# Kernel optimization log

Measured on AMD Instinct MI355X. Metric: run time of the kernel, lower is better.

## Reference

```python
import jax, jax.numpy as jnp
import numpy as np

V, D, T, H, L, B = 50257, 1024, 1024, 16, 6, 2
HS = D // H  # 64
EPS = 1e-5


def setup_inputs() -> dict:
    key = jax.random.key(0)
    ks = jax.random.split(key, 16)
    s = 0.02
    n = lambda k, sh: jax.random.normal(k, sh, jnp.float32) * s
    return {
        'idx': jax.random.randint(ks[0], (B, T), 0, V),
        'targets': jax.random.randint(ks[1], (B, T), 0, V),
        'tok_emb': n(ks[2], (V, D)),
        'pos_emb': n(ks[3], (T, D)),
        'wq': n(ks[4], (L, H, D, HS)),
        'wk': n(ks[5], (L, H, D, HS)),
        'wv': n(ks[6], (L, H, D, HS)),
        'wproj': n(ks[7], (L, D, D)),
        'bproj': jnp.zeros((L, D), jnp.float32),
        'ln1_g': jnp.ones((L, D), jnp.float32),
        'ln1_b': jnp.zeros((L, D), jnp.float32),
        'ln2_g': jnp.ones((L, D), jnp.float32),
        'ln2_b': jnp.zeros((L, D), jnp.float32),
        'w1': n(ks[8], (L, D, 4 * D)),
        'b1': jnp.zeros((L, 4 * D), jnp.float32),
        'w2': n(ks[9], (L, 4 * D, D)),
        'b2': jnp.zeros((L, D), jnp.float32),
        'lnf_g': jnp.ones((D,), jnp.float32),
        'lnf_b': jnp.zeros((D,), jnp.float32),
        'lm_w': n(ks[10], (D, V)),
        'lm_b': jnp.zeros((V,), jnp.float32),
    }


def _layernorm(x, g, b):
    mu = jnp.mean(x, axis=-1, keepdims=True)
    var = jnp.var(x, axis=-1, keepdims=True)
    return (x - mu) * jax.lax.rsqrt(var + EPS) * g + b


def _forward(idx, targets, tok_emb, pos_emb, wq, wk, wv, wproj, bproj,
             ln1_g, ln1_b, ln2_g, ln2_b, w1, b1, w2, b2, lnf_g, lnf_b, lm_w, lm_b):
    t = idx.shape[1]
    x = tok_emb[idx] + pos_emb[:t]  # [B,T,D]
    causal = jnp.tril(jnp.ones((t, t), bool))  # [T,T]
    neg_inf = jnp.float32(-jnp.inf)

    def block(x, p):
        (wq_l, wk_l, wv_l, wp_l, bp_l, g1, b1_ln, g2, b2_ln, wf1, bf1, wf2, bf2) = p
        h = _layernorm(x, g1, b1_ln)
        q = jnp.einsum('btd,hdk->bhtk', h, wq_l)
        k = jnp.einsum('btd,hdk->bhtk', h, wk_l)
        v = jnp.einsum('btd,hdk->bhtk', h, wv_l)
        scores = jnp.einsum('bhtk,bhsk->bhts', q, k) * (HS ** -0.5)
        scores = jnp.where(causal, scores, neg_inf)
        attn = jax.nn.softmax(scores, axis=-1)  # dropout p=0.0
        o = jnp.einsum('bhts,bhsk->bhtk', attn, v)
        o = o.transpose(0, 2, 1, 3).reshape(x.shape[0], t, H * HS)  # concat heads
        x = x + o @ wp_l + bp_l
        h2 = _layernorm(x, g2, b2_ln)
        x = x + jax.nn.relu(h2 @ wf1 + bf1) @ wf2 + bf2
        return x, None

    x, _ = jax.lax.scan(block, x, (wq, wk, wv, wproj, bproj,
                                   ln1_g, ln1_b, ln2_g, ln2_b, w1, b1, w2, b2))
    x = _layernorm(x, lnf_g, lnf_b)
    logits = x @ lm_w + lm_b  # [B,T,V]
    logp = jax.nn.log_softmax(logits, axis=-1)
    loss = -jnp.mean(jnp.take_along_axis(logp, targets[..., None], axis=-1))
    return logits, loss


def reference(idx, targets, tok_emb, pos_emb, wq, wk, wv, wproj, bproj,
              ln1_g, ln1_b, ln2_g, ln2_b, w1, b1, w2, b2, lnf_g, lnf_b, lm_w, lm_b):
    return _forward(idx, targets, tok_emb, pos_emb, wq, wk, wv, wproj, bproj,
                    ln1_g, ln1_b, ln2_g, ln2_b, w1, b1, w2, b2, lnf_g, lnf_b, lm_w, lm_b)
```

## Files before the change

kernel.cpp:

```cpp
#include <hip/hip_runtime.h>
#include <cstdint>
#include <cstddef>

typedef unsigned short u16;
typedef unsigned int u32;
typedef __bf16 bf16x8 __attribute__((ext_vector_type(8)));
typedef float f32x4 __attribute__((ext_vector_type(4)));
typedef short short8_t __attribute__((ext_vector_type(8)));

#define NV 50257
#define NVPAD 50304
#define NBLK_LM 393
#define PSTR 400
#define ND 1024
#define NT 1024
#define NH 16
#define NL 6
#define NB 2
#define NM 2048
#define NF 4096
#define EPSLN 1e-5f

__device__ __forceinline__ u16 f2bf(float f) {
    unsigned u = __float_as_uint(f);
    return (u16)((u + 0x7fffu + ((u >> 16) & 1u)) >> 16);
}
__device__ __forceinline__ float bf2f(u16 h) {
    return __uint_as_float(((unsigned)h) << 16);
}
__device__ __forceinline__ u32 pack2bf(float lo, float hi) {
    return (u32)f2bf(lo) | ((u32)f2bf(hi) << 16);
}

__device__ __forceinline__ void gload_lds16(const u16* g, u16* l) {
    __builtin_amdgcn_global_load_lds((const __attribute__((address_space(1))) void*)g,
                                     (__attribute__((address_space(3))) void*)l, 16, 0, 0);
}

__device__ __forceinline__ float wave_reduce_sum(float v) {
#pragma unroll
    for (int off = 32; off >= 1; off >>= 1) v += __shfl_xor(v, off, 64);
    return v;
}

__global__ __launch_bounds__(256) void k_embed(const int* __restrict__ idx,
                                               const float* __restrict__ tok,
                                               const float* __restrict__ pos,
                                               float* __restrict__ x) {
    int m = blockIdx.x;
    int t = m & (NT - 1);
    int tokid = idx[m];
    int d = threadIdx.x * 4;
    float4 a = *(const float4*)(tok + (size_t)tokid * ND + d);
    float4 p = *(const float4*)(pos + (size_t)t * ND + d);
    a.x += p.x; a.y += p.y; a.z += p.z; a.w += p.w;
    *(float4*)(x + (size_t)m * ND + d) = a;
}

__global__ __launch_bounds__(256) void k_layernorm(const float* __restrict__ x,
                                                   const float* __restrict__ g,
                                                   const float* __restrict__ b,
                                                   u16* __restrict__ outb) {
    int m = blockIdx.x;
    int d = threadIdx.x * 4;
    const float4 v = *(const float4*)(x + (size_t)m * ND + d);
    float s = v.x + v.y + v.z + v.w;
    float q = v.x * v.x + v.y * v.y + v.z * v.z + v.w * v.w;
    s = wave_reduce_sum(s);
    q = wave_reduce_sum(q);
    __shared__ float ss[4], sq[4];
    int lane = threadIdx.x & 63, w = threadIdx.x >> 6;
    if (lane == 0) { ss[w] = s; sq[w] = q; }
    __syncthreads();
    s = ss[0] + ss[1] + ss[2] + ss[3];
    q = sq[0] + sq[1] + sq[2] + sq[3];
    float mu = s * (1.0f / ND);
    float var = q * (1.0f / ND) - mu * mu;
    float rstd = rsqrtf(var + EPSLN);
    float4 gg = *(const float4*)(g + d);
    float4 bb = *(const float4*)(b + d);
    ushort4 pk;
    pk.x = f2bf((v.x - mu) * rstd * gg.x + bb.x);
    pk.y = f2bf((v.y - mu) * rstd * gg.y + bb.y);
    pk.z = f2bf((v.z - mu) * rstd * gg.z + bb.z);
    pk.w = f2bf((v.w - mu) * rstd * gg.w + bb.w);
    *(ushort4*)(outb + (size_t)m * ND + d) = pk;
}

__global__ __launch_bounds__(256) void k_wtrans(const float* __restrict__ W,
                                                u16* __restrict__ Wt,
                                                int K, int N, int Npad, int hs, int ld) {
    __shared__ float t[32][33];
    const int nb = blockIdx.x << 5, kb = blockIdx.y << 5;
    const int tx = threadIdx.x & 31, tq = threadIdx.x >> 5;
    const int n = nb + tx;
    if (n < N) {
        const int head = n / hs, nc = n - head * hs;
        const float* src = W + (size_t)head * K * hs + nc;
#pragma unroll
        for (int i = 0; i < 4; ++i)
            t[(tq << 2) + i][tx] = src[(size_t)(kb + (tq << 2) + i) * ld];
    } else {
#pragma unroll
        for (int i = 0; i < 4; ++i) t[(tq << 2) + i][tx] = 0.f;
    }
    __syncthreads();
#pragma unroll
    for (int i = 0; i < 4; ++i) {
        const int nn = nb + (tq << 2) + i;
        if (nn < Npad) Wt[(size_t)nn * K + kb + tx] = f2bf(t[tx][(tq << 2) + i]);
    }
}

__global__ __launch_bounds__(256) void k_wtrans_qkv(const float* __restrict__ Wq,
                                                    const float* __restrict__ Wk,
                                                    const float* __restrict__ Wv,
                                                    u16* __restrict__ Wt) {
    __shared__ float t[32][33];
    const float* W = (blockIdx.z == 0) ? Wq : (blockIdx.z == 1) ? Wk : Wv;
    u16* dst = Wt + (size_t)blockIdx.z * ND * ND;
    const int nb = blockIdx.x << 5, kb = blockIdx.y << 5;
    const int tx = threadIdx.x & 31, tq = threadIdx.x >> 5;
    const int n = nb + tx;
    {
        const int head = n >> 6, nc = n & 63;
        const float* src = W + (size_t)head * ND * 64 + nc;
#pragma unroll
        for (int i = 0; i < 4; ++i)
            t[(tq << 2) + i][tx] = src[(size_t)(kb + (tq << 2) + i) * 64];
    }
    __syncthreads();
#pragma unroll
    for (int i = 0; i < 4; ++i) {
        const int nn = nb + (tq << 2) + i;
        dst[(size_t)nn * ND + kb + tx] = f2bf(t[tx][(tq << 2) + i]);
    }
}

__global__ __launch_bounds__(256) void k_vtrans(const u16* __restrict__ qkv,
                                                u16* __restrict__ vt) {
    __shared__ u16 L[64][72];
    const int tt = blockIdx.x, bh = blockIdx.y;
    const int b = bh >> 4, h = bh & 15;
    const int tid = threadIdx.x;
    const int tr = tid >> 2, dc = (tid & 3) << 4;
    const u16* src = qkv + (size_t)(b * NT + tt * 64 + tr) * 3072 + 2048 + h * 64 + dc;
    short8_t v0 = *(const short8_t*)src;
    short8_t v1 = *(const short8_t*)(src + 8);
#pragma unroll
    for (int j = 0; j < 8; ++j) { L[tr][dc + j] = (u16)v0[j]; L[tr][dc + 8 + j] = (u16)v1[j]; }
    __syncthreads();
    const int dr = tid >> 2, tc = (tid & 3) << 4;
    union { u16 us[16]; short8_t v[2]; } tmp;
#pragma unroll
    for (int j = 0; j < 16; ++j) tmp.us[j] = L[tc + j][dr];
    u16* dst = vt + ((size_t)bh * 64 + dr) * NT + tt * 64 + tc;
    *(short8_t*)dst = tmp.v[0];
    *(short8_t*)(dst + 8) = tmp.v[1];
}

template <bool RELU, bool RESID, bool NBOUND, bool PART, bool OUTBF16>
__global__ __launch_bounds__(256) void k_mfma_gemm(
    const u16* __restrict__ A, const u16* __restrict__ Bt,
    const float* __restrict__ bias, const float* __restrict__ resid,
    float* __restrict__ Cf, u16* __restrict__ Cb,
    float* __restrict__ pmax_g, float* __restrict__ psum_g,
    int K, int N, int ldc)
{
    __shared__ u16 As[2][128 * 32];
    __shared__ u16 Bs[2][128 * 32];
    const int lin = blockIdx.y * 16 + blockIdx.x;
    const int nwg = (int)gridDim.y * 16;
    const int cpx = nwg >> 3;
    const int swz = (lin & 7) * cpx + (lin >> 3);
    const int m0 = (swz & 15) * 128;
    const int n0 = (swz >> 4) * 128;
    const int tid = threadIdx.x;
    const int lane = tid & 63, wv = tid >> 6;
    const int wr = wv >> 1, wc = wv & 1;
    const int lr = lane & 15, kg = lane >> 4;

    const int srow = lane >> 2;
    const int scol = (((lane & 3) ^ ((lane >> 3) & 3)) << 3);
    const u16* gA0 = A + (size_t)(m0 + wv * 16 + srow) * K + scol;
    const u16* gA1 = gA0 + (size_t)64 * K;
    const u16* gB0 = Bt + (size_t)(n0 + wv * 16 + srow) * K + scol;
    const u16* gB1 = gB0 + (size_t)64 * K;

    f32x4 acc[4][4] = {};
    const int nt = K >> 5;

    gload_lds16(gA0, &As[0][wv * 512]);
    gload_lds16(gA1, &As[0][2048 + wv * 512]);
    gload_lds16(gB0, &Bs[0][wv * 512]);
    gload_lds16(gB1, &Bs[0][2048 + wv * 512]);
    __syncthreads();

    int cur = 0;
    for (int t = 0; t < nt; ++t) {
        if (t + 1 < nt) {
            const int ko = (t + 1) << 5;
            gload_lds16(gA0 + ko, &As[cur ^ 1][wv * 512]);
            gload_lds16(gA1 + ko, &As[cur ^ 1][2048 + wv * 512]);
            gload_lds16(gB0 + ko, &Bs[cur ^ 1][wv * 512]);
            gload_lds16(gB1 + ko, &Bs[cur ^ 1][2048 + wv * 512]);
        }
        bf16x8 af[4], bfr[4];
        const int rsw = ((kg ^ ((lr >> 1) & 3)) << 3);
#pragma unroll
        for (int mi = 0; mi < 4; ++mi) {
            const int R = wr * 64 + mi * 16 + lr;
            af[mi] = *(const bf16x8*)&As[cur][R * 32 + rsw];
        }
#pragma unroll
        for (int ni = 0; ni < 4; ++ni) {
            const int R = wc * 64 + ni * 16 + lr;
            bfr[ni] = *(const bf16x8*)&Bs[cur][R * 32 + rsw];
        }
#pragma unroll
        for (int mi = 0; mi < 4; ++mi)
#pragma unroll
            for (int ni = 0; ni < 4; ++ni)
                acc[mi][ni] = __builtin_amdgcn_mfma_f32_16x16x32_bf16(af[mi], bfr[ni], acc[mi][ni], 0, 0, 0);
        __syncthreads();
        cur ^= 1;
    }
#pragma unroll
    for (int mi = 0; mi < 4; ++mi) {
#pragma unroll
        for (int ni = 0; ni < 4; ++ni) {
#pragma unroll
            for (int r = 0; r < 4; ++r) {
                const int row = m0 + wr * 64 + mi * 16 + kg * 4 + r;
                const int col = n0 + wc * 64 + ni * 16 + lr;
                if (NBOUND && col >= N) continue;
                float c = acc[mi][ni][r];
                if (bias) c += bias[col];
                if (RELU) c = fmaxf(c, 0.f);
                if (RESID) c += resid[(size_t)row * ldc + col];
                if (OUTBF16) Cb[(size_t)row * ldc + col] = f2bf(c);
                else         Cf[(size_t)row * ldc + col] = c;
            }
        }
    }
    if constexpr (PART) {
        __shared__ float redm[128][2];
        __shared__ float reds[128][2];
#pragma unroll
        for (int mi = 0; mi < 4; ++mi)
#pragma unroll
            for (int r = 0; r < 4; ++r) {
                float vmax = -3.0e38f;
#pragma unroll
                for (int ni = 0; ni < 4; ++ni) {
                    const int col = n0 + wc * 64 + ni * 16 + lr;
                    float c = acc[mi][ni][r] + ((col < N) ? bias[col] : 0.f);
                    if (col >= N) c = -3.0e38f;
                    vmax = fmaxf(vmax, c);
                }
                vmax = fmaxf(vmax, __shfl_xor(vmax, 1));
                vmax = fmaxf(vmax, __shfl_xor(vmax, 2));
                vmax = fmaxf(vmax, __shfl_xor(vmax, 4));
                vmax = fmaxf(vmax, __shfl_xor(vmax, 8));
                if (lr == 0) redm[wr * 64 + mi * 16 + kg * 4 + r][wc] = vmax;
            }
        __syncthreads();
#pragma unroll
        for (int mi = 0; mi < 4; ++mi)
#pragma unroll
            for (int r = 0; r < 4; ++r) {
                const int rloc = wr * 64 + mi * 16 + kg * 4 + r;
                const float M = fmaxf(redm[rloc][0], redm[rloc][1]);
                float s = 0.f;
#pragma unroll
                for (int ni = 0; ni < 4; ++ni) {
                    const int col = n0 + wc * 64 + ni * 16 + lr;
                    if (col < N) {
                        float c = acc[mi][ni][r] + bias[col];
                        s += __expf(c - M);
                    }
                }
                s += __shfl_xor(s, 1);
                s += __shfl_xor(s, 2);
                s += __shfl_xor(s, 4);
                s += __shfl_xor(s, 8);
                if (lr == 0) reds[rloc][wc] = s;
            }
        __syncthreads();
        if (tid < 128) {
            const float M = fmaxf(redm[tid][0], redm[tid][1]);
            const int nblk = n0 >> 7;
            pmax_g[(size_t)(m0 + tid) * PSTR + nblk] = M;
            psum_g[(size_t)(m0 + tid) * PSTR + nblk] = reds[tid][0] + reds[tid][1];
        }
    }
}

template <bool RELU, bool RESID, bool OUTBF16>
__global__ __launch_bounds__(256) void k_gemm_n64(
    const u16* __restrict__ A, const u16* __restrict__ Bt,
    const float* __restrict__ bias, const float* __restrict__ resid,
    float* __restrict__ Cf, u16* __restrict__ Cb,
    int K, int ldc)
{
    __shared__ u16 As[2][128 * 32];
    __shared__ u16 Bs[2][64 * 32];
    const int lin = blockIdx.y * 16 + blockIdx.x;
    const int nwg = (int)gridDim.y * 16;
    const int cpx = nwg >> 3;
    const int swz = (lin & 7) * cpx + (lin >> 3);
    const int m0 = (swz & 15) * 128;
    const int n0 = (swz >> 4) * 64;
    const int tid = threadIdx.x;
    const int lane = tid & 63, wv = tid >> 6;
    const int lr = lane & 15, kg = lane >> 4;

    const int srow = lane >> 2;
    const int scol = (((lane & 3) ^ ((lane >> 3) & 3)) << 3);
    const u16* gA0 = A + (size_t)(m0 + wv * 32 + srow) * K + scol;
    const u16* gA1 = gA0 + (size_t)16 * K;
    const u16* gB0 = Bt + (size_t)(n0 + wv * 16 + srow) * K + scol;

    f32x4 acc[2][4] = {};
    const int nt = K >> 5;

    gload_lds16(gA0, &As[0][wv * 1024]);
    gload_lds16(gA1, &As[0][wv * 1024 + 512]);
    gload_lds16(gB0, &Bs[0][wv * 512]);
    __syncthreads();

    int cur = 0;
    for (int t = 0; t < nt; ++t) {
        if (t + 1 < nt) {
            const int ko = (t + 1) << 5;
            gload_lds16(gA0 + ko, &As[cur ^ 1][wv * 1024]);
            gload_lds16(gA1 + ko, &As[cur ^ 1][wv * 1024 + 512]);
            gload_lds16(gB0 + ko, &Bs[cur ^ 1][wv * 512]);
        }
        bf16x8 af[2], bfr[4];
        const int rsw = ((kg ^ ((lr >> 1) & 3)) << 3);
#pragma unroll
        for (int mi = 0; mi < 2; ++mi)
            af[mi] = *(const bf16x8*)&As[cur][(wv * 32 + mi * 16 + lr) * 32 + rsw];
#pragma unroll
        for (int ni = 0; ni < 4; ++ni)
            bfr[ni] = *(const bf16x8*)&Bs[cur][(ni * 16 + lr) * 32 + rsw];
#pragma unroll
        for (int mi = 0; mi < 2; ++mi)
#pragma unroll
            for (int ni = 0; ni < 4; ++ni)
                acc[mi][ni] = __builtin_amdgcn_mfma_f32_16x16x32_bf16(af[mi], bfr[ni], acc[mi][ni], 0, 0, 0);
        __syncthreads();
        cur ^= 1;
    }
#pragma unroll
    for (int mi = 0; mi < 2; ++mi) {
#pragma unroll
        for (int ni = 0; ni < 4; ++ni) {
#pragma unroll
            for (int r = 0; r < 4; ++r) {
                const int row = m0 + wv * 32 + mi * 16 + kg * 4 + r;
                const int col = n0 + ni * 16 + lr;
                float c = acc[mi][ni][r];
                if (bias) c += bias[col];
                if (RELU) c = fmaxf(c, 0.f);
                if (RESID) c += resid[(size_t)row * ldc + col];
                if (OUTBF16) Cb[(size_t)row * ldc + col] = f2bf(c);
                else         Cf[(size_t)row * ldc + col] = c;
            }
        }
    }
}

__global__ __launch_bounds__(256) void k_attn_mfma(const u16* __restrict__ qkv,
                                                   const u16* __restrict__ vt,
                                                   u16* __restrict__ ob) {
    const int qt = blockIdx.x, bh = blockIdx.y;
    const int b = bh >> 4, h = bh & 15;
    const int tid = threadIdx.x;
    const int lane = tid & 63, w = tid >> 6;
    const int lr = lane & 15, kg = lane >> 4;

    __shared__ u16 Qs[64 * 64];
    __shared__ u16 Ks[2][64 * 64];
    __shared__ u16 Vs[2][64 * 64];

    const int srow8 = lane >> 3;
    const int csw = ((lane & 7) ^ srow8) << 3;

    {
        const int r0 = w * 8 + srow8;
        gload_lds16(qkv + (size_t)(b * NT + qt * 64 + r0) * 3072 + h * 64 + csw, &Qs[w * 512]);
        gload_lds16(qkv + (size_t)(b * NT + qt * 64 + 32 + r0) * 3072 + h * 64 + csw, &Qs[2048 + w * 512]);
    }
#define STAGE_KV(bb, st)                                                                            \
    {                                                                                               \
        const int r0_ = w * 8 + srow8;                                                              \
        gload_lds16(qkv + (size_t)(b * NT + (st) * 64 + r0_) * 3072 + 1024 + h * 64 + csw,          \
                    &Ks[bb][w * 512]);                                                              \
        gload_lds16(qkv + (size_t)(b * NT + (st) * 64 + 32 + r0_) * 3072 + 1024 + h * 64 + csw,     \
                    &Ks[bb][2048 + w * 512]);                                                       \
        gload_lds16(vt + ((size_t)bh * 64 + r0_) * NT + (st) * 64 + csw, &Vs[bb][w * 512]);         \
        gload_lds16(vt + ((size_t)bh * 64 + 32 + r0_) * NT + (st) * 64 + csw,                       \
                    &Vs[bb][2048 + w * 512]);                                                       \
    }
    STAGE_KV(0, 0);
    __syncthreads();

    bf16x8 qf[2];
    {
        const int qrow = w * 16 + lr;
#pragma unroll
        for (int ds_ = 0; ds_ < 2; ++ds_)
            qf[ds_] = *(const bf16x8*)&Qs[qrow * 64 + ((((ds_ << 2) + kg) ^ (lr & 7)) << 3)];
    }

    float mstate = -3.0e38f, lstate = 0.f;
    f32x4 acc_o[4] = {};
    const int qg = qt * 64 + w * 16 + lr;

    int cur = 0;
    for (int st = 0; st <= qt; ++st) {
        if (st < qt) STAGE_KV(cur ^ 1, st + 1);
        const bool diag = (st == qt);
        const int milim = diag ? w : 3;

        f32x4 acc_s[4] = {};
#pragma unroll
        for (int mi = 0; mi < 4; ++mi) {
            if (mi <= milim) {
                const int srw = mi * 16 + lr;
#pragma unroll
                for (int ds_ = 0; ds_ < 2; ++ds_) {
                    bf16x8 kf = *(const bf16x8*)&Ks[cur][srw * 64 + ((((ds_ << 2) + kg) ^ (lr & 7)) << 3)];
                    acc_s[mi] = __builtin_amdgcn_mfma_f32_16x16x32_bf16(kf, qf[ds_], acc_s[mi], 0, 0, 0);
                }
            }
        }
        float tilemax = -3.0e38f;
#pragma unroll
        for (int mi = 0; mi < 4; ++mi)
#pragma unroll
            for (int r = 0; r < 4; ++r) {
                float x_ = acc_s[mi][r] * 0.125f;
                const int sg = st * 64 + mi * 16 + kg * 4 + r;
                if (mi > milim || sg > qg) x_ = -3.0e38f;
                acc_s[mi][r] = x_;
                tilemax = fmaxf(tilemax, x_);
            }
        tilemax = fmaxf(tilemax, __shfl_xor(tilemax, 16));
        tilemax = fmaxf(tilemax, __shfl_xor(tilemax, 32));
        const float mnew = fmaxf(mstate, tilemax);
        const float rfac = __expf(mstate - mnew);
        mstate = mnew;

        float psum = 0.f;
        u32 pk[4][2];
#pragma unroll
        for (int mi = 0; mi < 4; ++mi) {
            float p0 = __expf(acc_s[mi][0] - mnew);
            float p1 = __expf(acc_s[mi][1] - mnew);
            float p2 = __expf(acc_s[mi][2] - mnew);
            float p3 = __expf(acc_s[mi][3] - mnew);
            psum += p0 + p1 + p2 + p3;
            pk[mi][0] = pack2bf(p0, p1);
            pk[mi][1] = pack2bf(p2, p3);
        }
        psum += __shfl_xor(psum, 16);
        psum += __shfl_xor(psum, 32);
        lstate = lstate * rfac + psum;

        float rf[4];
#pragma unroll
        for (int r = 0; r < 4; ++r) rf[r] = __shfl(rfac, kg * 4 + r);
#pragma unroll
        for (int ni = 0; ni < 4; ++ni)
#pragma unroll
            for (int r = 0; r < 4; ++r) acc_o[ni][r] *= rf[r];

        const int src0 = ((kg & 1) << 5) + lr;
        const int src1 = src0 + 16;
#pragma unroll
        for (int ks_ = 0; ks_ < 2; ++ks_) {
            const u32 lo_a = __shfl((int)pk[ks_ * 2][0], src0);
            const u32 lo_b = __shfl((int)pk[ks_ * 2][1], src0);
            const u32 lo_c = __shfl((int)pk[ks_ * 2][0], src1);
            const u32 lo_d = __shfl((int)pk[ks_ * 2][1], src1);
            const u32 hi_a = __shfl((int)pk[ks_ * 2 + 1][0], src0);
            const u32 hi_b = __shfl((int)pk[ks_ * 2 + 1][1], src0);
            const u32 hi_c = __shfl((int)pk[ks_ * 2 + 1][0], src1);
            const u32 hi_d = __shfl((int)pk[ks_ * 2 + 1][1], src1);
            union { u32 u[4]; bf16x8 v; } pa;
            pa.u[0] = (kg & 2) ? hi_a : lo_a;
            pa.u[1] = (kg & 2) ? hi_b : lo_b;
            pa.u[2] = (kg & 2) ? hi_c : lo_c;
            pa.u[3] = (kg & 2) ? hi_d : lo_d;
#pragma unroll
            for (int ni = 0; ni < 4; ++ni) {
                const int drow = ni * 16 + lr;
                bf16x8 vf = *(const bf16x8*)&Vs[cur][drow * 64 + ((((ks_ << 2) + kg) ^ (lr & 7)) << 3)];
                acc_o[ni] = __builtin_amdgcn_mfma_f32_16x16x32_bf16(pa.v, vf, acc_o[ni], 0, 0, 0);
            }
        }
        __syncthreads();
        cur ^= 1;
    }

    float il[4];
#pragma unroll
    for (int r = 0; r < 4; ++r) il[r] = 1.0f / __shfl(lstate, kg * 4 + r);
#pragma unroll
    for (int ni = 0; ni < 4; ++ni)
#pragma unroll
        for (int r = 0; r < 4; ++r) {
            const int q2 = qt * 64 + w * 16 + kg * 4 + r;
            ob[(size_t)(b * NT + q2) * ND + h * 64 + ni * 16 + lr] = f2bf(acc_o[ni][r] * il[r]);
        }
#undef STAGE_KV
}

__global__ __launch_bounds__(256) void k_losscombine(const float* __restrict__ pmax,
                                                     const float* __restrict__ psum,
                                                     const float* __restrict__ logits,
                                                     const int* __restrict__ targets,
                                                     float* __restrict__ rl) {
    const int row = blockIdx.x * 4 + (threadIdx.x >> 6);
    const int lane = threadIdx.x & 63;
    const float* pm = pmax + (size_t)row * PSTR;
    const float* ps = psum + (size_t)row * PSTR;
    float M = -3.0e38f;
    for (int j = lane; j < NBLK_LM; j += 64) M = fmaxf(M, pm[j]);
#pragma unroll
    for (int off = 32; off >= 1; off >>= 1) M = fmaxf(M, __shfl_xor(M, off, 64));
    float S = 0.f;
    for (int j = lane; j < NBLK_LM; j += 64) S += ps[j] * __expf(pm[j] - M);
    S = wave_reduce_sum(S);
    if (lane == 0)
        rl[row] = M + logf(S) - logits[(size_t)row * NV + targets[row]];
}

__global__ __launch_bounds__(256) void k_lossreduce(const float* __restrict__ rl,
                                                    float* __restrict__ out_loss) {
    int tid = threadIdx.x;
    float s = 0.f;
    for (int j = tid; j < NM; j += 256) s += rl[j];
    s = wave_reduce_sum(s);
    __shared__ float sv[4];
    int lane = tid & 63, w = tid >> 6;
    if (lane == 0) sv[w] = s;
    __syncthreads();
    if (tid == 0) out_loss[0] = (sv[0] + sv[1] + sv[2] + sv[3]) * (1.0f / NM);
}

extern "C" void kernel_launch(void* const* d_in, const int* in_sizes, int n_in,
                              void* d_out, int out_size, void* d_ws, size_t ws_size,
                              hipStream_t stream) {
    const int* idx      = (const int*)d_in[0];
    const int* targets  = (const int*)d_in[1];
    const float* tok    = (const float*)d_in[2];
    const float* pos    = (const float*)d_in[3];
    const float* wq     = (const float*)d_in[4];
    const float* wk     = (const float*)d_in[5];
    const float* wv     = (const float*)d_in[6];
    const float* wproj  = (const float*)d_in[7];
    const float* bproj  = (const float*)d_in[8];
    const float* ln1_g  = (const float*)d_in[9];
    const float* ln1_b  = (const float*)d_in[10];
    const float* ln2_g  = (const float*)d_in[11];
    const float* ln2_b  = (const float*)d_in[12];
    const float* w1     = (const float*)d_in[13];
    const float* b1     = (const float*)d_in[14];
    const float* w2     = (const float*)d_in[15];
    const float* b2     = (const float*)d_in[16];
    const float* lnf_g  = (const float*)d_in[17];
    const float* lnf_b  = (const float*)d_in[18];
    const float* lm_w   = (const float*)d_in[19];
    const float* lm_b   = (const float*)d_in[20];
    float* out = (float*)d_out;

    char* wsb = (char*)d_ws;
    auto alloc = [&](size_t bytes) { char* p = wsb; wsb += (bytes + 255) & ~(size_t)255; return p; };
    float* x     = (float*)alloc((size_t)NM * ND * 4);
    u16* h_bf    = (u16*)  alloc((size_t)NM * ND * 2);
    float* rl    = (float*)alloc((size_t)NM * 4);
    float* pmax  = (float*)alloc((size_t)NM * PSTR * 4);
    float* psum  = (float*)alloc((size_t)NM * PSTR * 4);
    char* region = (char*)alloc((size_t)NVPAD * ND * 2);
    u16* qkv_bf = (u16*)(region);
    u16* vt_bf  = (u16*)(region + ((size_t)12 << 20));
    u16* ob_bf  = (u16*)(region + ((size_t)16 << 20));
    u16* hid_bf = (u16*)(region + ((size_t)20 << 20));
    u16* wqkv_t = (u16*)(region + ((size_t)36 << 20));
    u16* wp_t   = (u16*)(region + ((size_t)42 << 20));
    u16* w1_t   = (u16*)(region + ((size_t)44 << 20));
    u16* w2_t   = (u16*)(region + ((size_t)52 << 20));
    u16* lm_t   = (u16*)(region);

    k_embed<<<NM, 256, 0, stream>>>(idx, tok, pos, x);

    for (int l = 0; l < NL; ++l) {
        const float* wq_l = wq + (size_t)l * NH * ND * 64;
        const float* wk_l = wk + (size_t)l * NH * ND * 64;
        const float* wv_l = wv + (size_t)l * NH * ND * 64;
        const float* wp_l = wproj + (size_t)l * ND * ND;
        const float* bp_l = bproj + (size_t)l * ND;
        const float* w1_l = w1 + (size_t)l * ND * NF;
        const float* b1_l = b1 + (size_t)l * NF;
        const float* w2_l = w2 + (size_t)l * NF * ND;
        const float* b2_l = b2 + (size_t)l * ND;

        k_layernorm<<<NM, 256, 0, stream>>>(x, ln1_g + (size_t)l * ND, ln1_b + (size_t)l * ND, h_bf);

        k_wtrans_qkv<<<dim3(32, 32, 3), 256, 0, stream>>>(wq_l, wk_l, wv_l, wqkv_t);
        k_mfma_gemm<false, false, false, false, true><<<dim3(16, 24), 256, 0, stream>>>(
            h_bf, wqkv_t, nullptr, nullptr, nullptr, qkv_bf, nullptr, nullptr, ND, 3 * ND, 3 * ND);

        k_vtrans<<<dim3(NT / 64, NB * NH), 256, 0, stream>>>(qkv_bf, vt_bf);
        k_attn_mfma<<<dim3(NT / 64, NB * NH), 256, 0, stream>>>(qkv_bf, vt_bf, ob_bf);

        k_wtrans<<<dim3(ND / 32, ND / 32), 256, 0, stream>>>(wp_l, wp_t, ND, ND, ND, ND, ND);
        k_gemm_n64<false, true, false><<<dim3(16, 16), 256, 0, stream>>>(
            ob_bf, wp_t, bp_l, x, x, nullptr, ND, ND);

        k_layernorm<<<NM, 256, 0, stream>>>(x, ln2_g + (size_t)l * ND, ln2_b + (size_t)l * ND, h_bf);

        k_wtrans<<<dim3(NF / 32, ND / 32), 256, 0, stream>>>(w1_l, w1_t, ND, NF, NF, NF, NF);
        k_mfma_gemm<true, false, false, false, true><<<dim3(16, 32), 256, 0, stream>>>(
            h_bf, w1_t, b1_l, nullptr, nullptr, hid_bf, nullptr, nullptr, ND, NF, NF);

        k_wtrans<<<dim3(ND / 32, NF / 32), 256, 0, stream>>>(w2_l, w2_t, NF, ND, ND, ND, ND);
        k_gemm_n64<false, true, false><<<dim3(16, 16), 256, 0, stream>>>(
            hid_bf, w2_t, b2_l, x, x, nullptr, NF, ND);
    }

    k_layernorm<<<NM, 256, 0, stream>>>(x, lnf_g, lnf_b, h_bf);

    k_wtrans<<<dim3(NVPAD / 32, ND / 32), 256, 0, stream>>>(lm_w, lm_t, ND, NV, NVPAD, NV, NV);
    k_mfma_gemm<false, false, true, true, false><<<dim3(16, NVPAD / 128), 256, 0, stream>>>(
        h_bf, lm_t, lm_b, nullptr, out, nullptr, pmax, psum, ND, NV, NV);

    k_losscombine<<<NM / 4, 256, 0, stream>>>(pmax, psum, out, targets, rl);
    k_lossreduce<<<1, 256, 0, stream>>>(rl, out + (size_t)NM * NV);
}
```

Baseline: 1.948 ms.

## Add 256x256 eight-wave LM-head GEMM with interleaved staging and fused softmax partials

Replaces the 128x128 LM-head GEMM with a dedicated 512-thread kernel that computes 256x256 tiles, stages with 64-wide K chunks through direct global-to-LDS loads, and interleaves loads with MFMA quadrants using barriers and priority hints. The softmax partial max/sum buffers are transposed to a block-major layout so the combine kernel reads them coalesced, and the unused template paths are dropped from the generic GEMM. Larger tiles cut global and LDS traffic per FLOP on the largest GEMM, at the cost of padding the vocabulary further and using 128 KB of LDS per block, which may limit occupancy.

```diff
diff --git a/kernel.cpp b/kernel.cpp
--- a/kernel.cpp
+++ b/kernel.cpp
@@ -9,9 +9,8 @@
 typedef short short8_t __attribute__((ext_vector_type(8)));
 
 #define NV 50257
-#define NVPAD 50304
-#define NBLK_LM 393
-#define PSTR 400
+#define NVPAD 50432
+#define NBLK_LM 197
 #define ND 1024
 #define NT 1024
 #define NH 16
@@ -159,12 +158,194 @@
     *(short8_t*)(dst + 8) = tmp.v[1];
 }
 
-template <bool RELU, bool RESID, bool NBOUND, bool PART, bool OUTBF16>
+__global__ __launch_bounds__(512, 2) void k_gemm8_lm(
+    const u16* __restrict__ A, const u16* __restrict__ Bt,
+    const float* __restrict__ bias,
+    float* __restrict__ Cf,
+    float* __restrict__ pmax_g, float* __restrict__ psum_g,
+    int K, int N, int ldc)
+{
+    __shared__ u16 As[2 * 256 * 64];
+    __shared__ u16 Bs[2 * 256 * 64];
+
+    const int nwg = (int)gridDim.x * (int)gridDim.y;
+    const int lin = (int)blockIdx.y * 8 + (int)blockIdx.x;
+    const int cpx = nwg >> 3;
+    const int swz = (lin & 7) * cpx + (lin >> 3);
+    const int m0 = (swz & 7) * 256;
+    const int n0 = (swz >> 3) * 256;
+
+    const int tid = threadIdx.x;
+    const int lane = tid & 63, w = tid >> 6;
+    const int wr = w >> 2, wc = w & 3;
+    const int lr = lane & 15, kg = lane >> 4;
+
+    const int srow = w * 8 + (lane >> 3);
+    const int scolu = ((lane & 7) ^ (lane >> 3)) << 3;
+    const u16* gA = A + (size_t)(m0 + srow) * K + scolu;
+    const u16* gB = Bt + (size_t)(n0 + srow) * K + scolu;
+
+    const int aoff = (wr * 128 + lr) * 64 + ((kg ^ (lr & 7)) << 3);
+    const int boff = (wc * 64 + lr) * 64 + ((kg ^ (lr & 7)) << 3);
+
+#define STG_A(buf, h, kt)                                                                   \
+    gload_lds16(gA + (size_t)((h) * 128) * K + (size_t)(kt) * 64,                           \
+                &As[(buf) * 16384 + (h) * 8192 + w * 512]);                                 \
+    gload_lds16(gA + (size_t)((h) * 128 + 64) * K + (size_t)(kt) * 64,                      \
+                &As[(buf) * 16384 + (h) * 8192 + 4096 + w * 512]);
+#define STG_B(buf, h, kt)                                                                   \
+    gload_lds16(gB + (size_t)((h) * 128) * K + (size_t)(kt) * 64,                           \
+                &Bs[(buf) * 16384 + (h) * 8192 + w * 512]);                                 \
+    gload_lds16(gB + (size_t)((h) * 128 + 64) * K + (size_t)(kt) * 64,                      \
+                &Bs[(buf) * 16384 + (h) * 8192 + 4096 + w * 512]);
+#define LDA(cur, mh, mi, ks) \
+    (*(const bf16x8*)&As[(cur) * 16384 + ((mh) * 64 + (mi) * 16) * 64 + (aoff ^ ((ks) << 5))])
+#define LDB(cur, nh, ni, ks) \
+    (*(const bf16x8*)&Bs[(cur) * 16384 + ((nh) * 32 + (ni) * 16) * 64 + (boff ^ ((ks) << 5))])
+
+    f32x4 acc[8][4] = {};
+    bf16x8 a[4][2], b[4][2];
+    const int nk = K >> 6;
+
+    STG_B(0, 0, 0);
+    STG_A(0, 0, 0);
+    STG_A(0, 1, 0);
+    STG_B(0, 1, 0);
+    STG_B(1, 0, 1);
+    STG_A(1, 0, 1);
+    asm volatile("s_waitcnt vmcnt(4)" ::: "memory");
+    __builtin_amdgcn_s_barrier();
+
+#define MFMA_Q(MI0, NI0)                                                                    \
+    _Pragma("unroll")                                                                       \
+    for (int mi = 0; mi < 4; ++mi) {                                                        \
+        _Pragma("unroll")                                                                   \
+        for (int ni = 0; ni < 2; ++ni) {                                                    \
+            acc[(MI0) + mi][(NI0) + ni] = __builtin_amdgcn_mfma_f32_16x16x32_bf16(          \
+                a[mi][0], b[(NI0) + ni][0], acc[(MI0) + mi][(NI0) + ni], 0, 0, 0);          \
+            acc[(MI0) + mi][(NI0) + ni] = __builtin_amdgcn_mfma_f32_16x16x32_bf16(          \
+                a[mi][1], b[(NI0) + ni][1], acc[(MI0) + mi][(NI0) + ni], 0, 0, 0);          \
+        }                                                                                   \
+    }
+
+    for (int t = 0; t < nk; ++t) {
+        const int cur = t & 1;
+        const int kt1 = (t + 1 < nk) ? t + 1 : 0;
+        const int kt2 = (t + 2 < nk) ? t + 2 : 0;
+
+#pragma unroll
+        for (int mi = 0; mi < 4; ++mi) { a[mi][0] = LDA(cur, 0, mi, 0); a[mi][1] = LDA(cur, 0, mi, 1); }
+#pragma unroll
+        for (int ni = 0; ni < 2; ++ni) { b[ni][0] = LDB(cur, 0, ni, 0); b[ni][1] = LDB(cur, 0, ni, 1); }
+        STG_A(cur ^ 1, 1, kt1);
+        __builtin_amdgcn_s_barrier();
+        __builtin_amdgcn_s_setprio(1);
+        MFMA_Q(0, 0);
+        __builtin_amdgcn_s_setprio(0);
+        __builtin_amdgcn_s_barrier();
+#pragma unroll
+        for (int ni = 0; ni < 2; ++ni) { b[2 + ni][0] = LDB(cur, 1, ni, 0); b[2 + ni][1] = LDB(cur, 1, ni, 1); }
+        STG_B(cur ^ 1, 1, kt1);
+        __builtin_amdgcn_s_barrier();
+        __builtin_amdgcn_s_setprio(1);
+        MFMA_Q(0, 2);
+        __builtin_amdgcn_s_setprio(0);
+        __builtin_amdgcn_s_barrier();
+#pragma unroll
+        for (int mi = 0; mi < 4; ++mi) { a[mi][0] = LDA(cur, 1, mi, 0); a[mi][1] = LDA(cur, 1, mi, 1); }
+        STG_B(cur, 0, kt2);
+        __builtin_amdgcn_s_barrier();
+        __builtin_amdgcn_s_setprio(1);
+        MFMA_Q(4, 2);
+        __builtin_amdgcn_s_setprio(0);
+        __builtin_amdgcn_s_barrier();
+        STG_A(cur, 0, kt2);
+        __builtin_amdgcn_s_barrier();
+        __builtin_amdgcn_s_setprio(1);
+        MFMA_Q(4, 0);
+        __builtin_amdgcn_s_setprio(0);
+        asm volatile("s_waitcnt vmcnt(4)" ::: "memory");
+        __builtin_amdgcn_s_barrier();
+    }
+    asm volatile("s_waitcnt vmcnt(0)" ::: "memory");
+    __builtin_amdgcn_s_barrier();
+
+#pragma unroll
+    for (int q = 0; q < 8; ++q) {
+#pragma unroll
+        for (int ni = 0; ni < 4; ++ni) {
+#pragma unroll
+            for (int r = 0; r < 4; ++r) {
+                const int row = m0 + wr * 128 + q * 16 + kg * 4 + r;
+                const int col = n0 + wc * 64 + ni * 16 + lr;
+                if (col >= N) continue;
+                Cf[(size_t)row * ldc + col] = acc[q][ni][r] + bias[col];
+            }
+        }
+    }
+
+    float* redm = (float*)As;
+    float* reds = redm + 1024;
+#pragma unroll
+    for (int q = 0; q < 8; ++q) {
+#pragma unroll
+        for (int r = 0; r < 4; ++r) {
+            float vmax = -3.0e38f;
+#pragma unroll
+            for (int ni = 0; ni < 4; ++ni) {
+                const int col = n0 + wc * 64 + ni * 16 + lr;
+                float c = (col < N) ? (acc[q][ni][r] + bias[col]) : -3.0e38f;
+                vmax = fmaxf(vmax, c);
+            }
+            vmax = fmaxf(vmax, __shfl_xor(vmax, 1));
+            vmax = fmaxf(vmax, __shfl_xor(vmax, 2));
+            vmax = fmaxf(vmax, __shfl_xor(vmax, 4));
+            vmax = fmaxf(vmax, __shfl_xor(vmax, 8));
+            if (lr == 0) redm[wc * 256 + wr * 128 + q * 16 + kg * 4 + r] = vmax;
+        }
+    }
+    __syncthreads();
+#pragma unroll
+    for (int q = 0; q < 8; ++q) {
+#pragma unroll
+        for (int r = 0; r < 4; ++r) {
+            const int rloc = wr * 128 + q * 16 + kg * 4 + r;
+            const float M = fmaxf(fmaxf(redm[rloc], redm[256 + rloc]),
+                                  fmaxf(redm[512 + rloc], redm[768 + rloc]));
+            float s = 0.f;
+#pragma unroll
+            for (int ni = 0; ni < 4; ++ni) {
+                const int col = n0 + wc * 64 + ni * 16 + lr;
+                if (col < N) s += __expf(acc[q][ni][r] + bias[col] - M);
+            }
+            s += __shfl_xor(s, 1);
+            s += __shfl_xor(s, 2);
+            s += __shfl_xor(s, 4);
+            s += __shfl_xor(s, 8);
+            if (lr == 0) reds[wc * 256 + rloc] = s;
+        }
+    }
+    __syncthreads();
+    if (tid < 256) {
+        const float M = fmaxf(fmaxf(redm[tid], redm[256 + tid]),
+                              fmaxf(redm[512 + tid], redm[768 + tid]));
+        const float S = reds[tid] + reds[256 + tid] + reds[512 + tid] + reds[768 + tid];
+        const int nblk = n0 >> 8;
+        pmax_g[(size_t)nblk * NM + m0 + tid] = M;
+        psum_g[(size_t)nblk * NM + m0 + tid] = S;
+    }
+#undef STG_A
+#undef STG_B
+#undef LDA
+#undef LDB
+#undef MFMA_Q
+}
+
+template <bool RELU, bool OUTBF16>
 __global__ __launch_bounds__(256) void k_mfma_gemm(
     const u16* __restrict__ A, const u16* __restrict__ Bt,
-    const float* __restrict__ bias, const float* __restrict__ resid,
+    const float* __restrict__ bias,
     float* __restrict__ Cf, u16* __restrict__ Cb,
-    float* __restrict__ pmax_g, float* __restrict__ psum_g,
     int K, int N, int ldc)
 {
     __shared__ u16 As[2][128 * 32];
@@ -233,65 +414,12 @@
             for (int r = 0; r < 4; ++r) {
                 const int row = m0 + wr * 64 + mi * 16 + kg * 4 + r;
                 const int col = n0 + wc * 64 + ni * 16 + lr;
-                if (NBOUND && col >= N) continue;
                 float c = acc[mi][ni][r];
                 if (bias) c += bias[col];
                 if (RELU) c = fmaxf(c, 0.f);
-                if (RESID) c += resid[(size_t)row * ldc + col];
                 if (OUTBF16) Cb[(size_t)row * ldc + col] = f2bf(c);
                 else         Cf[(size_t)row * ldc + col] = c;
             }
-        }
-    }
-    if constexpr (PART) {
-        __shared__ float redm[128][2];
-        __shared__ float reds[128][2];
-#pragma unroll
-        for (int mi = 0; mi < 4; ++mi)
-#pragma unroll
-            for (int r = 0; r < 4; ++r) {
-                float vmax = -3.0e38f;
-#pragma unroll
-                for (int ni = 0; ni < 4; ++ni) {
-                    const int col = n0 + wc * 64 + ni * 16 + lr;
-                    float c = acc[mi][ni][r] + ((col < N) ? bias[col] : 0.f);
-                    if (col >= N) c = -3.0e38f;
-                    vmax = fmaxf(vmax, c);
-                }
-                vmax = fmaxf(vmax, __shfl_xor(vmax, 1));
-                vmax = fmaxf(vmax, __shfl_xor(vmax, 2));
-                vmax = fmaxf(vmax, __shfl_xor(vmax, 4));
-                vmax = fmaxf(vmax, __shfl_xor(vmax, 8));
-                if (lr == 0) redm[wr * 64 + mi * 16 + kg * 4 + r][wc] = vmax;
-            }
-        __syncthreads();
-#pragma unroll
-        for (int mi = 0; mi < 4; ++mi)
-#pragma unroll
-            for (int r = 0; r < 4; ++r) {
-                const int rloc = wr * 64 + mi * 16 + kg * 4 + r;
-                const float M = fmaxf(redm[rloc][0], redm[rloc][1]);
-                float s = 0.f;
-#pragma unroll
-                for (int ni = 0; ni < 4; ++ni) {
-                    const int col = n0 + wc * 64 + ni * 16 + lr;
-                    if (col < N) {
-                        float c = acc[mi][ni][r] + bias[col];
-                        s += __expf(c - M);
-                    }
-                }
-                s += __shfl_xor(s, 1);
-                s += __shfl_xor(s, 2);
-                s += __shfl_xor(s, 4);
-                s += __shfl_xor(s, 8);
-                if (lr == 0) reds[rloc][wc] = s;
-            }
-        __syncthreads();
-        if (tid < 128) {
-            const float M = fmaxf(redm[tid][0], redm[tid][1]);
-            const int nblk = n0 >> 7;
-            pmax_g[(size_t)(m0 + tid) * PSTR + nblk] = M;
-            psum_g[(size_t)(m0 + tid) * PSTR + nblk] = reds[tid][0] + reds[tid][1];
         }
     }
 }
@@ -526,14 +654,13 @@
                                                      float* __restrict__ rl) {
     const int row = blockIdx.x * 4 + (threadIdx.x >> 6);
     const int lane = threadIdx.x & 63;
-    const float* pm = pmax + (size_t)row * PSTR;
-    const float* ps = psum + (size_t)row * PSTR;
     float M = -3.0e38f;
-    for (int j = lane; j < NBLK_LM; j += 64) M = fmaxf(M, pm[j]);
+    for (int j = lane; j < NBLK_LM; j += 64) M = fmaxf(M, pmax[(size_t)j * NM + row]);
 #pragma unroll
     for (int off = 32; off >= 1; off >>= 1) M = fmaxf(M, __shfl_xor(M, off, 64));
     float S = 0.f;
-    for (int j = lane; j < NBLK_LM; j += 64) S += ps[j] * __expf(pm[j] - M);
+    for (int j = lane; j < NBLK_LM; j += 64)
+        S += psum[(size_t)j * NM + row] * __expf(pmax[(size_t)j * NM + row] - M);
     S = wave_reduce_sum(S);
     if (lane == 0)
         rl[row] = M + logf(S) - logits[(size_t)row * NV + targets[row]];
@@ -583,8 +710,8 @@
     float* x     = (float*)alloc((size_t)NM * ND * 4);
     u16* h_bf    = (u16*)  alloc((size_t)NM * ND * 2);
     float* rl    = (float*)alloc((size_t)NM * 4);
-    float* pmax  = (float*)alloc((size_t)NM * PSTR * 4);
-    float* psum  = (float*)alloc((size_t)NM * PSTR * 4);
+    float* pmax  = (float*)alloc((size_t)NBLK_LM * NM * 4);
+    float* psum  = (float*)alloc((size_t)NBLK_LM * NM * 4);
     char* region = (char*)alloc((size_t)NVPAD * ND * 2);
     u16* qkv_bf = (u16*)(region);
     u16* vt_bf  = (u16*)(region + ((size_t)12 << 20));
@@ -612,8 +739,8 @@
         k_layernorm<<<NM, 256, 0, stream>>>(x, ln1_g + (size_t)l * ND, ln1_b + (size_t)l * ND, h_bf);
 
         k_wtrans_qkv<<<dim3(32, 32, 3), 256, 0, stream>>>(wq_l, wk_l, wv_l, wqkv_t);
-        k_mfma_gemm<false, false, false, false, true><<<dim3(16, 24), 256, 0, stream>>>(
-            h_bf, wqkv_t, nullptr, nullptr, nullptr, qkv_bf, nullptr, nullptr, ND, 3 * ND, 3 * ND);
+        k_mfma_gemm<false, true><<<dim3(16, 24), 256, 0, stream>>>(
+            h_bf, wqkv_t, nullptr, nullptr, qkv_bf, ND, 3 * ND, 3 * ND);
 
         k_vtrans<<<dim3(NT / 64, NB * NH), 256, 0, stream>>>(qkv_bf, vt_bf);
         k_attn_mfma<<<dim3(NT / 64, NB * NH), 256, 0, stream>>>(qkv_bf, vt_bf, ob_bf);
@@ -625,8 +752,8 @@
         k_layernorm<<<NM, 256, 0, stream>>>(x, ln2_g + (size_t)l * ND, ln2_b + (size_t)l * ND, h_bf);
 
         k_wtrans<<<dim3(NF / 32, ND / 32), 256, 0, stream>>>(w1_l, w1_t, ND, NF, NF, NF, NF);
-        k_mfma_gemm<true, false, false, false, true><<<dim3(16, 32), 256, 0, stream>>>(
-            h_bf, w1_t, b1_l, nullptr, nullptr, hid_bf, nullptr, nullptr, ND, NF, NF);
+        k_mfma_gemm<true, true><<<dim3(16, 32), 256, 0, stream>>>(
+            h_bf, w1_t, b1_l, nullptr, hid_bf, ND, NF, NF);
 
         k_wtrans<<<dim3(ND / 32, NF / 32), 256, 0, stream>>>(w2_l, w2_t, NF, ND, ND, ND, ND);
         k_gemm_n64<false, true, false><<<dim3(16, 16), 256, 0, stream>>>(
@@ -636,8 +763,8 @@
     k_layernorm<<<NM, 256, 0, stream>>>(x, lnf_g, lnf_b, h_bf);
 
     k_wtrans<<<dim3(NVPAD / 32, ND / 32), 256, 0, stream>>>(lm_w, lm_t, ND, NV, NVPAD, NV, NV);
-    k_mfma_gemm<false, false, true, true, false><<<dim3(16, NVPAD / 128), 256, 0, stream>>>(
-        h_bf, lm_t, lm_b, nullptr, out, nullptr, pmax, psum, ND, NV, NV);
+    k_gemm8_lm<<<dim3(8, NVPAD / 256), 512, 0, stream>>>(
+        h_bf, lm_t, lm_b, out, pmax, psum, ND, NV, NV);
 
     k_losscombine<<<NM / 4, 256, 0, stream>>>(pmax, psum, out, targets, rl);
     k_lossreduce<<<1, 256, 0, stream>>>(rl, out + (size_t)NM * NV);
```

Result: no change. 1.952 ms (+0.2%).

## Deepen GEMM and attention LDS pipelines with vmcnt-based multi-stage prefetch

Applied to the files above, without the earlier changes.

The two GEMM kernels move from a double-buffered LDS pipeline with a full __syncthreads per K-step to a 4-stage ring that prefetches 3 tiles ahead. Each step does one barrier gated by explicit s_waitcnt vmcnt counts. Attention K/V staging goes from 2 to 3 buffers with the same scheme. The partial max/sum buffers for the LM-head loss are transposed to block-major layout and reuse LDS. This aims to hide global-load latency and cut barrier stalls, at the cost of more LDS per workgroup, which may lower occupancy. The hand-counted vmcnt values must match the number of outstanding loads exactly.

```diff
diff --git a/kernel.cpp b/kernel.cpp
--- a/kernel.cpp
+++ b/kernel.cpp
@@ -11,7 +11,6 @@
 #define NV 50257
 #define NVPAD 50304
 #define NBLK_LM 393
-#define PSTR 400
 #define ND 1024
 #define NT 1024
 #define NH 16
@@ -20,6 +19,8 @@
 #define NM 2048
 #define NF 4096
 #define EPSLN 1e-5f
+
+#define VMCNT(n) asm volatile("s_waitcnt vmcnt(" #n ")" ::: "memory")
 
 __device__ __forceinline__ u16 f2bf(float f) {
     unsigned u = __float_as_uint(f);
@@ -159,16 +160,16 @@
     *(short8_t*)(dst + 8) = tmp.v[1];
 }
 
-template <bool RELU, bool RESID, bool NBOUND, bool PART, bool OUTBF16>
-__global__ __launch_bounds__(256) void k_mfma_gemm(
+template <bool RELU, bool NBOUND, bool PART, bool OUTBF16>
+__global__ __launch_bounds__(256) void k_gemm128(
     const u16* __restrict__ A, const u16* __restrict__ Bt,
-    const float* __restrict__ bias, const float* __restrict__ resid,
+    const float* __restrict__ bias,
     float* __restrict__ Cf, u16* __restrict__ Cb,
     float* __restrict__ pmax_g, float* __restrict__ psum_g,
     int K, int N, int ldc)
 {
-    __shared__ u16 As[2][128 * 32];
-    __shared__ u16 Bs[2][128 * 32];
+    __shared__ u16 As[4][128 * 32];
+    __shared__ u16 Bs[4][128 * 32];
     const int lin = blockIdx.y * 16 + blockIdx.x;
     const int nwg = (int)gridDim.y * 16;
     const int cpx = nwg >> 3;
@@ -187,44 +188,46 @@
     const u16* gB0 = Bt + (size_t)(n0 + wv * 16 + srow) * K + scol;
     const u16* gB1 = gB0 + (size_t)64 * K;
 
+#define STG128(buf, kt)                                                   \
+    gload_lds16(gA0 + (size_t)(kt) * 32, &As[buf][wv * 512]);             \
+    gload_lds16(gA1 + (size_t)(kt) * 32, &As[buf][2048 + wv * 512]);      \
+    gload_lds16(gB0 + (size_t)(kt) * 32, &Bs[buf][wv * 512]);             \
+    gload_lds16(gB1 + (size_t)(kt) * 32, &Bs[buf][2048 + wv * 512]);
+
     f32x4 acc[4][4] = {};
     const int nt = K >> 5;
 
-    gload_lds16(gA0, &As[0][wv * 512]);
-    gload_lds16(gA1, &As[0][2048 + wv * 512]);
-    gload_lds16(gB0, &Bs[0][wv * 512]);
-    gload_lds16(gB1, &Bs[0][2048 + wv * 512]);
-    __syncthreads();
-
-    int cur = 0;
+    STG128(0, 0);
+    STG128(1, 1);
+    STG128(2, 2);
+
     for (int t = 0; t < nt; ++t) {
-        if (t + 1 < nt) {
-            const int ko = (t + 1) << 5;
-            gload_lds16(gA0 + ko, &As[cur ^ 1][wv * 512]);
-            gload_lds16(gA1 + ko, &As[cur ^ 1][2048 + wv * 512]);
-            gload_lds16(gB0 + ko, &Bs[cur ^ 1][wv * 512]);
-            gload_lds16(gB1 + ko, &Bs[cur ^ 1][2048 + wv * 512]);
-        }
+        if (t < nt - 2)       { VMCNT(8); }
+        else if (t == nt - 2) { VMCNT(4); }
+        else                  { VMCNT(0); }
+        __builtin_amdgcn_s_barrier();
+        if (t + 3 < nt) { STG128((t + 3) & 3, t + 3); }
+
+        const int tb = t & 3;
         bf16x8 af[4], bfr[4];
         const int rsw = ((kg ^ ((lr >> 1) & 3)) << 3);
 #pragma unroll
         for (int mi = 0; mi < 4; ++mi) {
             const int R = wr * 64 + mi * 16 + lr;
-            af[mi] = *(const bf16x8*)&As[cur][R * 32 + rsw];
+            af[mi] = *(const bf16x8*)&As[tb][R * 32 + rsw];
         }
 #pragma unroll
         for (int ni = 0; ni < 4; ++ni) {
             const int R = wc * 64 + ni * 16 + lr;
-            bfr[ni] = *(const bf16x8*)&Bs[cur][R * 32 + rsw];
+            bfr[ni] = *(const bf16x8*)&Bs[tb][R * 32 + rsw];
         }
 #pragma unroll
         for (int mi = 0; mi < 4; ++mi)
 #pragma unroll
             for (int ni = 0; ni < 4; ++ni)
                 acc[mi][ni] = __builtin_amdgcn_mfma_f32_16x16x32_bf16(af[mi], bfr[ni], acc[mi][ni], 0, 0, 0);
-        __syncthreads();
-        cur ^= 1;
-    }
+    }
+
 #pragma unroll
     for (int mi = 0; mi < 4; ++mi) {
 #pragma unroll
@@ -237,15 +240,16 @@
                 float c = acc[mi][ni][r];
                 if (bias) c += bias[col];
                 if (RELU) c = fmaxf(c, 0.f);
-                if (RESID) c += resid[(size_t)row * ldc + col];
                 if (OUTBF16) Cb[(size_t)row * ldc + col] = f2bf(c);
                 else         Cf[(size_t)row * ldc + col] = c;
             }
         }
     }
+
     if constexpr (PART) {
-        __shared__ float redm[128][2];
-        __shared__ float reds[128][2];
+        __syncthreads();
+        float* redm = (float*)&As[0][0];
+        float* reds = redm + 256;
 #pragma unroll
         for (int mi = 0; mi < 4; ++mi)
 #pragma unroll
@@ -254,15 +258,14 @@
 #pragma unroll
                 for (int ni = 0; ni < 4; ++ni) {
                     const int col = n0 + wc * 64 + ni * 16 + lr;
-                    float c = acc[mi][ni][r] + ((col < N) ? bias[col] : 0.f);
-                    if (col >= N) c = -3.0e38f;
+                    float c = (col < N) ? (acc[mi][ni][r] + bias[col]) : -3.0e38f;
                     vmax = fmaxf(vmax, c);
                 }
                 vmax = fmaxf(vmax, __shfl_xor(vmax, 1));
                 vmax = fmaxf(vmax, __shfl_xor(vmax, 2));
                 vmax = fmaxf(vmax, __shfl_xor(vmax, 4));
                 vmax = fmaxf(vmax, __shfl_xor(vmax, 8));
-                if (lr == 0) redm[wr * 64 + mi * 16 + kg * 4 + r][wc] = vmax;
+                if (lr == 0) redm[wc * 128 + wr * 64 + mi * 16 + kg * 4 + r] = vmax;
             }
         __syncthreads();
 #pragma unroll
@@ -270,30 +273,29 @@
 #pragma unroll
             for (int r = 0; r < 4; ++r) {
                 const int rloc = wr * 64 + mi * 16 + kg * 4 + r;
-                const float M = fmaxf(redm[rloc][0], redm[rloc][1]);
+                const float M = fmaxf(redm[rloc], redm[128 + rloc]);
                 float s = 0.f;
 #pragma unroll
                 for (int ni = 0; ni < 4; ++ni) {
                     const int col = n0 + wc * 64 + ni * 16 + lr;
-                    if (col < N) {
-                        float c = acc[mi][ni][r] + bias[col];
-                        s += __expf(c - M);
-                    }
+                    if (col < N) s += __expf(acc[mi][ni][r] + bias[col] - M);
                 }
                 s += __shfl_xor(s, 1);
                 s += __shfl_xor(s, 2);
                 s += __shfl_xor(s, 4);
                 s += __shfl_xor(s, 8);
-                if (lr == 0) reds[rloc][wc] = s;
+                if (lr == 0) reds[wc * 128 + rloc] = s;
             }
         __syncthreads();
         if (tid < 128) {
-            const float M = fmaxf(redm[tid][0], redm[tid][1]);
+            const float M = fmaxf(redm[tid], redm[128 + tid]);
+            const float S = reds[tid] + reds[128 + tid];
             const int nblk = n0 >> 7;
-            pmax_g[(size_t)(m0 + tid) * PSTR + nblk] = M;
-            psum_g[(size_t)(m0 + tid) * PSTR + nblk] = reds[tid][0] + reds[tid][1];
-        }
-    }
+            pmax_g[(size_t)nblk * NM + m0 + tid] = M;
+            psum_g[(size_t)nblk * NM + m0 + tid] = S;
+        }
+    }
+#undef STG128
 }
 
 template <bool RELU, bool RESID, bool OUTBF16>
@@ -303,8 +305,8 @@
     float* __restrict__ Cf, u16* __restrict__ Cb,
     int K, int ldc)
 {
-    __shared__ u16 As[2][128 * 32];
-    __shared__ u16 Bs[2][64 * 32];
+    __shared__ u16 As[4][128 * 32];
+    __shared__ u16 Bs[4][64 * 32];
     const int lin = blockIdx.y * 16 + blockIdx.x;
     const int nwg = (int)gridDim.y * 16;
     const int cpx = nwg >> 3;
@@ -321,38 +323,41 @@
     const u16* gA1 = gA0 + (size_t)16 * K;
     const u16* gB0 = Bt + (size_t)(n0 + wv * 16 + srow) * K + scol;
 
+#define STGN64(buf, kt)                                                   \
+    gload_lds16(gA0 + (size_t)(kt) * 32, &As[buf][wv * 1024]);            \
+    gload_lds16(gA1 + (size_t)(kt) * 32, &As[buf][wv * 1024 + 512]);      \
+    gload_lds16(gB0 + (size_t)(kt) * 32, &Bs[buf][wv * 512]);
+
     f32x4 acc[2][4] = {};
     const int nt = K >> 5;
 
-    gload_lds16(gA0, &As[0][wv * 1024]);
-    gload_lds16(gA1, &As[0][wv * 1024 + 512]);
-    gload_lds16(gB0, &Bs[0][wv * 512]);
-    __syncthreads();
-
-    int cur = 0;
+    STGN64(0, 0);
+    STGN64(1, 1);
+    STGN64(2, 2);
+
     for (int t = 0; t < nt; ++t) {
-        if (t + 1 < nt) {
-            const int ko = (t + 1) << 5;
-            gload_lds16(gA0 + ko, &As[cur ^ 1][wv * 1024]);
-            gload_lds16(gA1 + ko, &As[cur ^ 1][wv * 1024 + 512]);
-            gload_lds16(gB0 + ko, &Bs[cur ^ 1][wv * 512]);
-        }
+        if (t < nt - 2)       { VMCNT(6); }
+        else if (t == nt - 2) { VMCNT(3); }
+        else                  { VMCNT(0); }
+        __builtin_amdgcn_s_barrier();
+        if (t + 3 < nt) { STGN64((t + 3) & 3, t + 3); }
+
+        const int tb = t & 3;
         bf16x8 af[2], bfr[4];
         const int rsw = ((kg ^ ((lr >> 1) & 3)) << 3);
 #pragma unroll
         for (int mi = 0; mi < 2; ++mi)
-            af[mi] = *(const bf16x8*)&As[cur][(wv * 32 + mi * 16 + lr) * 32 + rsw];
+            af[mi] = *(const bf16x8*)&As[tb][(wv * 32 + mi * 16 + lr) * 32 + rsw];
 #pragma unroll
         for (int ni = 0; ni < 4; ++ni)
-            bfr[ni] = *(const bf16x8*)&Bs[cur][(ni * 16 + lr) * 32 + rsw];
+            bfr[ni] = *(const bf16x8*)&Bs[tb][(ni * 16 + lr) * 32 + rsw];
 #pragma unroll
         for (int mi = 0; mi < 2; ++mi)
 #pragma unroll
             for (int ni = 0; ni < 4; ++ni)
                 acc[mi][ni] = __builtin_amdgcn_mfma_f32_16x16x32_bf16(af[mi], bfr[ni], acc[mi][ni], 0, 0, 0);
-        __syncthreads();
-        cur ^= 1;
-    }
+    }
+
 #pragma unroll
     for (int mi = 0; mi < 2; ++mi) {
 #pragma unroll
@@ -370,6 +375,7 @@
             }
         }
     }
+#undef STGN64
 }
 
 __global__ __launch_bounds__(256) void k_attn_mfma(const u16* __restrict__ qkv,
@@ -382,8 +388,8 @@
     const int lr = lane & 15, kg = lane >> 4;
 
     __shared__ u16 Qs[64 * 64];
-    __shared__ u16 Ks[2][64 * 64];
-    __shared__ u16 Vs[2][64 * 64];
+    __shared__ u16 Ks[3][64 * 64];
+    __shared__ u16 Vs[3][64 * 64];
 
     const int srow8 = lane >> 3;
     const int csw = ((lane & 7) ^ srow8) << 3;
@@ -405,7 +411,9 @@
                     &Vs[bb][2048 + w * 512]);                                                       \
     }
     STAGE_KV(0, 0);
-    __syncthreads();
+    if (qt >= 1) STAGE_KV(1, 1);
+    if (qt == 0) { VMCNT(0); } else { VMCNT(4); }
+    __builtin_amdgcn_s_barrier();
 
     bf16x8 qf[2];
     {
@@ -421,7 +429,14 @@
 
     int cur = 0;
     for (int st = 0; st <= qt; ++st) {
-        if (st < qt) STAGE_KV(cur ^ 1, st + 1);
+        if (st > 0) {
+            if (st < qt) { VMCNT(4); } else { VMCNT(0); }
+            __builtin_amdgcn_s_barrier();
+        }
+        if (st + 2 <= qt) {
+            int tgt = cur + 2; if (tgt >= 3) tgt -= 3;
+            STAGE_KV(tgt, st + 2);
+        }
         const bool diag = (st == qt);
         const int milim = diag ? w : 3;
 
@@ -502,8 +517,7 @@
                 acc_o[ni] = __builtin_amdgcn_mfma_f32_16x16x32_bf16(pa.v, vf, acc_o[ni], 0, 0, 0);
             }
         }
-        __syncthreads();
-        cur ^= 1;
+        cur = (cur == 2) ? 0 : cur + 1;
     }
 
     float il[4];
@@ -526,14 +540,13 @@
                                                      float* __restrict__ rl) {
     const int row = blockIdx.x * 4 + (threadIdx.x >> 6);
     const int lane = threadIdx.x & 63;
-    const float* pm = pmax + (size_t)row * PSTR;
-    const float* ps = psum + (size_t)row * PSTR;
     float M = -3.0e38f;
-    for (int j = lane; j < NBLK_LM; j += 64) M = fmaxf(M, pm[j]);
+    for (int j = lane; j < NBLK_LM; j += 64) M = fmaxf(M, pmax[(size_t)j * NM + row]);
 #pragma unroll
     for (int off = 32; off >= 1; off >>= 1) M = fmaxf(M, __shfl_xor(M, off, 64));
     float S = 0.f;
-    for (int j = lane; j < NBLK_LM; j += 64) S += ps[j] * __expf(pm[j] - M);
+    for (int j = lane; j < NBLK_LM; j += 64)
+        S += psum[(size_t)j * NM + row] * __expf(pmax[(size_t)j * NM + row] - M);
     S = wave_reduce_sum(S);
     if (lane == 0)
         rl[row] = M + logf(S) - logits[(size_t)row * NV + targets[row]];
@@ -583,8 +596,8 @@
     float* x     = (float*)alloc((size_t)NM * ND * 4);
     u16* h_bf    = (u16*)  alloc((size_t)NM * ND * 2);
     float* rl    = (float*)alloc((size_t)NM * 4);
-    float* pmax  = (float*)alloc((size_t)NM * PSTR * 4);
-    float* psum  = (float*)alloc((size_t)NM * PSTR * 4);
+    float* pmax  = (float*)alloc((size_t)NBLK_LM * NM * 4);
+    float* psum  = (float*)alloc((size_t)NBLK_LM * NM * 4);
     char* region = (char*)alloc((size_t)NVPAD * ND * 2);
     u16* qkv_bf = (u16*)(region);
     u16* vt_bf  = (u16*)(region + ((size_t)12 << 20));
@@ -612,8 +625,8 @@
         k_layernorm<<<NM, 256, 0, stream>>>(x, ln1_g + (size_t)l * ND, ln1_b + (size_t)l * ND, h_bf);
 
         k_wtrans_qkv<<<dim3(32, 32, 3), 256, 0, stream>>>(wq_l, wk_l, wv_l, wqkv_t);
-        k_mfma_gemm<false, false, false, false, true><<<dim3(16, 24), 256, 0, stream>>>(
-            h_bf, wqkv_t, nullptr, nullptr, nullptr, qkv_bf, nullptr, nullptr, ND, 3 * ND, 3 * ND);
+        k_gemm128<false, false, false, true><<<dim3(16, 24), 256, 0, stream>>>(
+            h_bf, wqkv_t, nullptr, nullptr, qkv_bf, nullptr, nullptr, ND, 3 * ND, 3 * ND);
 
         k_vtrans<<<dim3(NT / 64, NB * NH), 256, 0, stream>>>(qkv_bf, vt_bf);
         k_attn_mfma<<<dim3(NT / 64, NB * NH), 256, 0, stream>>>(qkv_bf, vt_bf, ob_bf);
@@ -625,8 +638,8 @@
         k_layernorm<<<NM, 256, 0, stream>>>(x, ln2_g + (size_t)l * ND, ln2_b + (size_t)l * ND, h_bf);
 
         k_wtrans<<<dim3(NF / 32, ND / 32), 256, 0, stream>>>(w1_l, w1_t, ND, NF, NF, NF, NF);
-        k_mfma_gemm<true, false, false, false, true><<<dim3(16, 32), 256, 0, stream>>>(
-            h_bf, w1_t, b1_l, nullptr, nullptr, hid_bf, nullptr, nullptr, ND, NF, NF);
+        k_gemm128<true, false, false, true><<<dim3(16, 32), 256, 0, stream>>>(
+            h_bf, w1_t, b1_l, nullptr, hid_bf, nullptr, nullptr, ND, NF, NF);
 
         k_wtrans<<<dim3(ND / 32, NF / 32), 256, 0, stream>>>(w2_l, w2_t, NF, ND, ND, ND, ND);
         k_gemm_n64<false, true, false><<<dim3(16, 16), 256, 0, stream>>>(
@@ -636,8 +649,8 @@
     k_layernorm<<<NM, 256, 0, stream>>>(x, lnf_g, lnf_b, h_bf);
 
     k_wtrans<<<dim3(NVPAD / 32, ND / 32), 256, 0, stream>>>(lm_w, lm_t, ND, NV, NVPAD, NV, NV);
-    k_mfma_gemm<false, false, true, true, false><<<dim3(16, NVPAD / 128), 256, 0, stream>>>(
-        h_bf, lm_t, lm_b, nullptr, out, nullptr, pmax, psum, ND, NV, NV);
+    k_gemm128<false, true, true, false><<<dim3(16, NVPAD / 128), 256, 0, stream>>>(
+        h_bf, lm_t, lm_b, out, nullptr, pmax, psum, ND, NV, NV);
 
     k_losscombine<<<NM / 4, 256, 0, stream>>>(pmax, psum, out, targets, rl);
     k_lossreduce<<<1, 256, 0, stream>>>(rl, out + (size_t)NM * NV);
```

Result: slower. 2.120 ms (+8.9%).
